# Optimization experiments

Hardware: AMD Instinct MI355X
Metric: run time of the kernel (lower is better)

Reference implementation:

```python
import jax, jax.numpy as jnp
import numpy as np

SC = np.float32(np.sqrt(0.5))


def _reflect_idx(l, m):
    # symmetric-extension gather indices for a length-l axis padded by m each side
    x = np.arange(-m, l + m, dtype=np.float64)
    minx, maxx = -0.5, l - 0.5
    rng = maxx - minx
    mod = np.fmod(x - minx, 2.0 * rng)
    mod = np.where(mod < 0, mod + 2.0 * rng, mod)
    out = np.where(mod >= rng, 2.0 * rng - mod, mod) + minx
    return out.astype(np.int32)


def _conv_h(X, h):
    # true 'valid' convolution (filter flipped, as np.convolve) along H of (N,C,H,W)
    k = h.shape[0]
    w = jnp.flip(h).reshape(1, 1, k, 1).astype(X.dtype)
    N, C, H, W = X.shape
    y = jax.lax.conv_general_dilated(X.reshape(N * C, 1, H, W), w, (1, 1), 'VALID',
                                     dimension_numbers=('NCHW', 'OIHW', 'NCHW'))
    return y.reshape(N, C, -1, W)


def colfilter(X, h):
    # odd-tap filter along rows (H) with symmetric padding, output same H
    m = h.shape[0] // 2
    xe = _reflect_idx(X.shape[2], m)
    return _conv_h(X[:, :, xe], h)


def rowfilter(X, h):
    return colfilter(X.transpose(0, 1, 3, 2), h).transpose(0, 1, 3, 2)


def colifilt(X, ha, hb, highpass):
    # Polyphase form of dtcwt's colifilt: four phase outputs interleaved into 2*H rows.
    N, C, r, W = X.shape
    m = ha.shape[0]
    m2 = m // 2
    xe = _reflect_idx(r, m2)  # len r + m
    hao, hae = ha[0::2], ha[1::2]
    hbo, hbe = hb[0::2], hb[1::2]
    if m2 % 2 == 0:
        t = np.arange(3, r + m, 2)
        off = 2
    else:
        t = np.arange(2, r + m - 1, 2)
        off = 0
    # highpass pairs have sum(ha*hb) < 0 -> swapped quarter-sample phases
    ta, tb = (t - 1, t) if highpass else (t, t - 1)
    Xb = X[:, :, xe[tb - off]]
    Xa = X[:, :, xe[ta - off]]
    Xb2 = X[:, :, xe[tb]] if off else Xb
    Xa2 = X[:, :, xe[ta]] if off else Xa
    y0 = _conv_h(Xb, hao)
    y1 = _conv_h(Xa, hbo)
    y2 = _conv_h(Xb2, hae)
    y3 = _conv_h(Xa2, hbe)
    Y = jnp.stack([y0, y1, y2, y3], axis=3)  # (N,C,r/2,4,W)
    return Y.reshape(N, C, 2 * r, W)


def rowifilt(X, ha, hb, highpass):
    return colifilt(X.transpose(0, 1, 3, 2), ha, hb, highpass).transpose(0, 1, 3, 2)


def c2q(w1, w2):
    # complex orientation pair (N,C,h,w,2) -> real quad image (N,C,2h,2w)
    w1r, w1i = w1[..., 0], w1[..., 1]
    w2r, w2i = w2[..., 0], w2[..., 1]
    x1 = (w1r + w2r) * SC  # top-left
    x2 = (w1i + w2i) * SC  # top-right
    x3 = (w1i - w2i) * SC  # bottom-left
    x4 = (w2r - w1r) * SC  # bottom-right
    N, C, H, W = x1.shape
    top = jnp.stack([x1, x2], axis=-1).reshape(N, C, H, 2 * W)
    bot = jnp.stack([x3, x4], axis=-1).reshape(N, C, H, 2 * W)
    return jnp.stack([top, bot], axis=3).reshape(N, C, 2 * H, 2 * W)


def _bands(yh):
    lh = c2q(yh[:, :, 0], yh[:, :, 5])
    hl = c2q(yh[:, :, 2], yh[:, :, 3])
    hh = c2q(yh[:, :, 1], yh[:, :, 4])
    return lh, hl, hh


def _crop(ll, ref):
    if ll.shape[2] != ref.shape[2]:
        ll = ll[:, :, 1:-1]
    if ll.shape[3] != ref.shape[3]:
        ll = ll[:, :, :, 1:-1]
    return ll


def _inv_j2plus(ll, yh, g0a, g0b, g1a, g1b):
    lh, hl, hh = _bands(yh)
    ll = _crop(ll, lh)
    y1 = colifilt(ll, g0b, g0a, False) + colifilt(lh, g1b, g1a, True)
    y2 = colifilt(hl, g0b, g0a, False) + colifilt(hh, g1b, g1a, True)
    return rowifilt(y1, g0b, g0a, False) + rowifilt(y2, g1b, g1a, True)


def _inv_j1(ll, yh, g0o, g1o):
    lh, hl, hh = _bands(yh)
    ll = _crop(ll, lh)
    y1 = colfilter(ll, g0o) + colfilter(lh, g1o)
    y2 = colfilter(hl, g0o) + colfilter(hh, g1o)
    return rowfilter(y1, g0o) + rowfilter(y2, g1o)


def _filters():
    # near_sym_a (5,7)-tap biorthogonal synthesis filters
    g0o = np.array([-3.0, -15.0, 73.0, 170.0, 73.0, -15.0, -3.0]) / 280.0
    g1o = np.array([-1.0, -5.0, 12.0, -5.0, -1.0]) / 20.0
    # qshift_06 10-tap quarter-shift filters
    h0a = np.array([0.03516384, 0.0, -0.08832942, 0.23389032, 0.76027237,
                    0.58751830, 0.0, -0.11430184, 0.0, 0.0])
    g0b = h0a
    g0a = h0a[::-1]
    g1a = h0a * np.array([1.0, -1.0] * 5)
    g1b = g1a[::-1]
    f32 = lambda a: jnp.asarray(np.ascontiguousarray(a), dtype=jnp.float32)
    return f32(g0o), f32(g1o), f32(g0a), f32(g0b), f32(g1a), f32(g1b)


def setup_inputs():
    key = jax.random.key(0)
    k1, k2, k3, k4 = jax.random.split(key, 4)
    N, C = 4, 64
    yl = jax.random.normal(k1, (N, C, 64, 64), dtype=jnp.float32)
    yh1 = jax.random.normal(k2, (N, C, 6, 128, 128, 2), dtype=jnp.float32)
    yh2 = jax.random.normal(k3, (N, C, 6, 64, 64, 2), dtype=jnp.float32)
    yh3 = jax.random.normal(k4, (N, C, 6, 32, 32, 2), dtype=jnp.float32)
    g0o, g1o, g0a, g0b, g1a, g1b = _filters()
    return {"yl": yl, "yh1": yh1, "yh2": yh2, "yh3": yh3,
            "g0o": g0o, "g1o": g1o, "g0a": g0a, "g0b": g0b, "g1a": g1a, "g1b": g1b}


def reference(yl, yh1, yh2, yh3, g0o, g1o, g0a, g0b, g1a, g1b):
    ll = _inv_j2plus(yl, yh3, g0a, g0b, g1a, g1b)   # 64 -> 128
    ll = _inv_j2plus(ll, yh2, g0a, g0b, g1a, g1b)   # 128 -> 256
    return _inv_j1(ll, yh1, g0o, g1o)               # 256 -> 256
```

## Files before the change

### kernel.cpp

```cpp
#include <hip/hip_runtime.h>

#define SC 0.70710678118654752440f

typedef _Float16 h4v __attribute__((ext_vector_type(4)));
typedef _Float16 h8v __attribute__((ext_vector_type(8)));

__device__ __forceinline__ float rfl(float x) {
    return __int_as_float(__builtin_amdgcn_readfirstlane(__float_as_int(x)));
}

__device__ __forceinline__ float4 ld4(const float* __restrict__ p) {
    return *(const float4*)p;
}
__device__ __forceinline__ float4 ld4(const _Float16* __restrict__ p) {
    h4v h = *(const h4v*)p;
    return make_float4((float)h[0], (float)h[1], (float)h[2], (float)h[3]);
}
__device__ __forceinline__ void st4(float* __restrict__ p, float4 v) {
    *(float4*)p = v;
}
__device__ __forceinline__ void st4(_Float16* __restrict__ p, float4 v) {
    h4v h;
    h[0] = (_Float16)v.x; h[1] = (_Float16)v.y;
    h[2] = (_Float16)v.z; h[3] = (_Float16)v.w;
    *(h4v*)p = h;
}

__device__ __forceinline__ h8v pack8(float4 a, float4 b) {
    h8v h;
    h[0] = (_Float16)a.x; h[1] = (_Float16)a.y;
    h[2] = (_Float16)a.z; h[3] = (_Float16)a.w;
    h[4] = (_Float16)b.x; h[5] = (_Float16)b.y;
    h[6] = (_Float16)b.z; h[7] = (_Float16)b.w;
    return h;
}
__device__ __forceinline__ void unpack8(h8v h, bool rv, float4& y1, float4& y2) {
    float4 p = make_float4((float)h[0], (float)h[1], (float)h[2], (float)h[3]);
    float4 q = make_float4((float)h[4], (float)h[5], (float)h[6], (float)h[7]);
    float4 pr = make_float4(p.w, p.z, p.y, p.x);
    float4 qr = make_float4(q.w, q.z, q.y, q.x);
    y1 = rv ? pr : p;
    y2 = rv ? qr : q;
}

__device__ __forceinline__ int reflFull(int p, int n) {
    int x = max(p, ~p);
    return min(x, 2 * n - 1 - x);
}
__device__ __forceinline__ int pairRefl(int t, int NP, bool& sw) {
    int x = max(t, ~t);
    int tp = min(x, 2 * NP - 1 - x);
    sw = (tp != t);
    return tp;
}

__device__ __forceinline__ constexpr int cflIdx(int s, int k) {
    return (s == 0) ? 8 - 2 * k : (s == 1) ? 1 + 2 * k : (s == 2) ? 9 - 2 * k : 2 * k;
}
__device__ __forceinline__ constexpr int cfhIdx(int s, int k) {
    return (s == 0) ? 1 + 2 * k : (s == 1) ? 8 - 2 * k : (s == 2) ? 2 * k : 9 - 2 * k;
}

__device__ __forceinline__ float4 f4fma(float c, float4 a, float4 acc) {
    return make_float4(fmaf(c, a.x, acc.x), fmaf(c, a.y, acc.y),
                       fmaf(c, a.z, acc.z), fmaf(c, a.w, acc.w));
}
__device__ __forceinline__ float4 f4sel(bool sw, float4 a, float4 b) {
    return sw ? a : b;
}

struct Band4 { float4 e05, o05, e23, o23, e14, o14; };

__device__ __forceinline__ Band4 loadBands4(const float* __restrict__ bp, int HW2,
                                            int boff, bool sw) {
    float4 B0 = *(const float4*)(bp + 0 * HW2 + boff);
    float4 B1 = *(const float4*)(bp + 1 * HW2 + boff);
    float4 B2 = *(const float4*)(bp + 2 * HW2 + boff);
    float4 B3 = *(const float4*)(bp + 3 * HW2 + boff);
    float4 B4 = *(const float4*)(bp + 4 * HW2 + boff);
    float4 B5 = *(const float4*)(bp + 5 * HW2 + boff);
    float4 ve05 = {B0.x + B5.x, B0.y + B5.y, B0.z + B5.z, B0.w + B5.w};
    float4 vo05 = {B0.y - B5.y, B5.x - B0.x, B0.w - B5.w, B5.z - B0.z};
    float4 ve23 = {B2.x + B3.x, B2.y + B3.y, B2.z + B3.z, B2.w + B3.w};
    float4 vo23 = {B2.y - B3.y, B3.x - B2.x, B2.w - B3.w, B3.z - B2.z};
    float4 ve14 = {B1.x + B4.x, B1.y + B4.y, B1.z + B4.z, B1.w + B4.w};
    float4 vo14 = {B1.y - B4.y, B4.x - B1.x, B1.w - B4.w, B4.z - B1.z};
    Band4 r;
    r.e05 = f4sel(sw, vo05, ve05);  r.o05 = f4sel(sw, ve05, vo05);
    r.e23 = f4sel(sw, vo23, ve23);  r.o23 = f4sel(sw, ve23, vo23);
    r.e14 = f4sel(sw, vo14, ve14);  r.o14 = f4sel(sw, ve14, vo14);
    return r;
}

template <int N> struct Log2 { static constexpr int v = 1 + Log2<N / 2>::v; };
template <> struct Log2<1> { static constexpr int v = 0; };

template <int H, int W, bool BND, typename TIn, typename SY>
__device__ __forceinline__ void j2_colstage(
        const TIn* __restrict__ llp, const float* __restrict__ bp,
        const float* G0, const float* G1, SY& sY, int tid, int q0) {
    constexpr int LOGW = Log2<W>::v;
    constexpr int U4 = W / 2, LOGU4 = LOGW - 1;
    constexpr int r = 2 * H, LOGC2 = LOGW + 1;
    constexpr int HW2 = H * W * 2;
    int u4 = tid & (U4 - 1);
    int qq = tid >> LOGU4;
    int q = q0 + qq;
    float4 A1[4], A1b[4], A2[4];
#pragma unroll
    for (int s = 0; s < 4; ++s) {
        A1[s] = {0, 0, 0, 0}; A1b[s] = {0, 0, 0, 0}; A2[s] = {0, 0, 0, 0};
    }
#pragma unroll
    for (int k = 0; k < 5; ++k) {
        int t = q + k - 2;
        int pe, po, tp; bool sw;
        if constexpr (BND) {
            pe = reflFull(2 * t, r);
            po = reflFull(2 * t + 1, r);
            tp = pairRefl(t, H, sw);
        } else {
            pe = 2 * t; po = 2 * t + 1; tp = t; sw = false;
        }
        float4 lle = ld4(llp + ((pe << LOGC2) + 4 * u4));
        float4 llo = ld4(llp + ((po << LOGC2) + 4 * u4));
        Band4 B = loadBands4(bp, HW2, (tp << (LOGW + 1)) + 4 * u4, sw);
#pragma unroll
        for (int s = 0; s < 4; ++s) {
            float4 lv  = (s & 1) ? llo   : lle;
            float4 v05 = (s & 1) ? B.e05 : B.o05;
            float4 v23 = (s & 1) ? B.o23 : B.e23;
            float4 v14 = (s & 1) ? B.e14 : B.o14;
            float c0 = G0[cflIdx(s, k)];
            float c1 = G1[cfhIdx(s, k)];
            A1[s]  = f4fma(c0, lv,  A1[s]);
            A1b[s] = f4fma(c1, v05, A1b[s]);
            A2[s]  = f4fma(c0, v23, f4fma(c1, v14, A2[s]));
        }
    }
#pragma unroll
    for (int s = 0; s < 4; ++s) {
        float4 w1 = f4fma(SC, A1b[s], A1[s]);
        float4 w2 = {SC * A2[s].x, SC * A2[s].y, SC * A2[s].z, SC * A2[s].w};
        sY[4 * qq + s][u4] = pack8(w1, w2);
    }
}

template <int H, int W, typename TIn, typename TOut>
__global__ __launch_bounds__(256) void j2_fused(
        const TIn* __restrict__ ll, const float* __restrict__ yh,
        const float* __restrict__ g0b, const float* __restrict__ g1a,
        TOut* __restrict__ out) {
    constexpr int LOGW = Log2<W>::v;
    constexpr int U4 = W / 2, LOGU4 = LOGW - 1;
    constexpr int QI = 256 / U4;
    constexpr int TI = 4 * QI;
    constexpr int r = 2 * H, COUT = 4 * W;
    constexpr int HW2 = H * W * 2;
    constexpr int NCH = W / 2;
    __shared__ h8v sY[TI][NCH + 1];

    const int tid = threadIdx.x;
    const int nc = blockIdx.y;
    const int q0 = blockIdx.x * QI;
    const TIn* llp = ll + (size_t)nc * r * (2 * W);
    const float* bp  = yh + (size_t)nc * 6 * HW2;

    float G0[10], G1[10];
#pragma unroll
    for (int i = 0; i < 10; ++i) { G0[i] = rfl(g0b[i]); G1[i] = rfl(g1a[i]); }

    if (q0 >= 2 && q0 + QI + 2 <= H)
        j2_colstage<H, W, false>(llp, bp, G0, G1, sY, tid, q0);
    else
        j2_colstage<H, W, true>(llp, bp, G0, G1, sY, tid, q0);
    __syncthreads();

    TOut* op = out + (size_t)nc * (4 * H) * COUT;
#pragma unroll
    for (int v = 0; v < (TI * W) / 512; ++v) {
        int lin = v * 256 + tid;
        int uc = lin & (U4 - 1);
        int il = lin >> LOGU4;
        float e1[6], o1[6], e2[6], o2[6];
#pragma unroll
        for (int d = 0; d < 3; ++d) {
            int a = uc - 1 + d;
            int ac = reflFull(a, NCH);
            bool rv = (ac != a);
            float4 y1, y2;
            unpack8(sY[il][ac], rv, y1, y2);
            e1[2 * d] = y1.x;  o1[2 * d] = y1.y;
            e1[2 * d + 1] = y1.z;  o1[2 * d + 1] = y1.w;
            e2[2 * d] = y2.x;  o2[2 * d] = y2.y;
            e2[2 * d + 1] = y2.z;  o2[2 * d + 1] = y2.w;
        }
        float acc[8];
#pragma unroll
        for (int b = 0; b < 2; ++b)
#pragma unroll
            for (int s = 0; s < 4; ++s) {
                float a = 0.f;
#pragma unroll
                for (int k = 0; k < 5; ++k) {
                    int m = b + k;
                    float v1 = (s & 1) ? o1[m] : e1[m];
                    float v2 = (s & 1) ? e2[m] : o2[m];
                    a = fmaf(G0[cflIdx(s, k)], v1, a);
                    a = fmaf(G1[cfhIdx(s, k)], v2, a);
                }
                acc[4 * b + s] = a;
            }
        int grow = 4 * q0 + il;
        st4(op + (size_t)grow * COUT + 8 * uc,
            make_float4(acc[0], acc[1], acc[2], acc[3]));
        st4(op + (size_t)grow * COUT + 8 * uc + 4,
            make_float4(acc[4], acc[5], acc[6], acc[7]));
    }
}

template <int H, int W, bool BND, typename TIn, typename SY>
__device__ __forceinline__ void j1_colstage(
        const TIn* __restrict__ llp, const float* __restrict__ bp,
        const float* g0f, const float* g1f, SY& sY, int tid, int qi0) {
    constexpr int LOGW = Log2<W>::v;
    constexpr int U4 = W / 2, LOGU4 = LOGW - 1;
    constexpr int r = 2 * H, LOGC2 = LOGW + 1;
    constexpr int HW2 = H * W * 2;
    int u4 = tid & (U4 - 1);
    int qq = tid >> LOGU4;
    int qi = qi0 + qq;
    float4 A1[4], A1b[4], A2[4];
#pragma unroll
    for (int s = 0; s < 4; ++s) {
        A1[s] = {0, 0, 0, 0}; A1b[s] = {0, 0, 0, 0}; A2[s] = {0, 0, 0, 0};
    }
#pragma unroll
    for (int rr = 0; rr < 10; ++rr) {
        int praw = 4 * qi - 3 + rr;
        int p = BND ? reflFull(praw, r) : praw;
        float4 v = ld4(llp + ((p << LOGC2) + 4 * u4));
#pragma unroll
        for (int di = 0; di < 4; ++di) {
            int k = rr - di;
            if (k >= 0 && k <= 6) A1[di] = f4fma(g0f[k], v, A1[di]);
        }
    }
#pragma unroll
    for (int tr = 0; tr < 6; ++tr) {
        int t = 2 * qi - 2 + tr;
        int tp; bool sw;
        if constexpr (BND) tp = pairRefl(t, H, sw);
        else { tp = t; sw = false; }
        Band4 B = loadBands4(bp, HW2, (tp << (LOGW + 1)) + 4 * u4, sw);
#pragma unroll
        for (int di = 0; di < 4; ++di) {
            int k1e = 2 * tr - di - 2;
            int k1o = k1e + 1;
            int k0e = 2 * tr - di - 1;
            int k0o = k0e + 1;
            if (k1e >= 0 && k1e <= 4) {
                A1b[di] = f4fma(g1f[k1e], B.e05, A1b[di]);
                A2[di]  = f4fma(g1f[k1e], B.e14, A2[di]);
            }
            if (k1o >= 0 && k1o <= 4) {
                A1b[di] = f4fma(g1f[k1o], B.o05, A1b[di]);
                A2[di]  = f4fma(g1f[k1o], B.o14, A2[di]);
            }
            if (k0e >= 0 && k0e <= 6) A2[di] = f4fma(g0f[k0e], B.e23, A2[di]);
            if (k0o >= 0 && k0o <= 6) A2[di] = f4fma(g0f[k0o], B.o23, A2[di]);
        }
    }
#pragma unroll
    for (int di = 0; di < 4; ++di) {
        float4 w1 = f4fma(SC, A1b[di], A1[di]);
        float4 w2 = {SC * A2[di].x, SC * A2[di].y, SC * A2[di].z, SC * A2[di].w};
        sY[4 * qq + di][u4] = pack8(w1, w2);
    }
}

template <int H, int W, typename TIn>
__global__ __launch_bounds__(256) void j1_fused(
        const TIn* __restrict__ ll, const float* __restrict__ yh,
        const float* __restrict__ g0o, const float* __restrict__ g1o,
        float* __restrict__ out) {
    constexpr int LOGW = Log2<W>::v;
    constexpr int U4 = W / 2, LOGU4 = LOGW - 1;
    constexpr int QI = 256 / U4;
    constexpr int TI = 4 * QI;
    constexpr int r = 2 * H, c = 2 * W;
    constexpr int HW2 = H * W * 2;
    constexpr int NCH = W / 2;
    __shared__ h8v sY[TI][NCH + 1];

    const int tid = threadIdx.x;
    const int nc = blockIdx.y;
    const int qi0 = blockIdx.x * QI;
    const TIn* llp = ll + (size_t)nc * r * c;
    const float* bp  = yh + (size_t)nc * 6 * HW2;

    float g0f[7], g1f[5];
#pragma unroll
    for (int k = 0; k < 7; ++k) g0f[k] = rfl(g0o[6 - k]);
#pragma unroll
    for (int k = 0; k < 5; ++k) g1f[k] = rfl(g1o[4 - k]);

    if (qi0 >= 1 && 2 * (qi0 + QI) + 4 <= H && 4 * (qi0 + QI) + 7 <= r)
        j1_colstage<H, W, false>(llp, bp, g0f, g1f, sY, tid, qi0);
    else
        j1_colstage<H, W, true>(llp, bp, g0f, g1f, sY, tid, qi0);
    __syncthreads();

    float* op = out + (size_t)nc * r * c;
#pragma unroll
    for (int v = 0; v < (TI * W) / 1024; ++v) {
        int lin = v * 256 + tid;
        int g8 = lin & (W / 4 - 1);
        int il = lin >> (LOGW - 2);
        float e1[8], o1[8], e2[8], o2[8];
#pragma unroll
        for (int d = 0; d < 4; ++d) {
            int a = 2 * g8 - 1 + d;
            int ac = reflFull(a, NCH);
            bool rv = (ac != a);
            float4 y1, y2;
            unpack8(sY[il][ac], rv, y1, y2);
            e1[2 * d] = y1.x;  o1[2 * d] = y1.y;
            e1[2 * d + 1] = y1.z;  o1[2 * d + 1] = y1.w;
            e2[2 * d] = y2.x;  o2[2 * d] = y2.y;
            e2[2 * d + 1] = y2.z;  o2[2 * d + 1] = y2.w;
        }
        float acc[8];
#pragma unroll
        for (int b = 0; b < 2; ++b)
#pragma unroll
            for (int s = 0; s < 4; ++s) {
                float a = 0.f;
#pragma unroll
                for (int k = 0; k < 7; ++k) {
                    int rel = s + k + 1;
                    int mm = (rel >> 1) + 2 * b;
                    a = fmaf(g0f[k], (rel & 1) ? o1[mm] : e1[mm], a);
                }
#pragma unroll
                for (int k = 0; k < 5; ++k) {
                    int rel = s + k + 2;
                    int mm = (rel >> 1) + 2 * b;
                    a = fmaf(g1f[k], (rel & 1) ? o2[mm] : e2[mm], a);
                }
                acc[4 * b + s] = a;
            }
        int grow = 4 * qi0 + il;
        *(float4*)(op + (size_t)grow * c + 8 * g8) =
            make_float4(acc[0], acc[1], acc[2], acc[3]);
        *(float4*)(op + (size_t)grow * c + 8 * g8 + 4) =
            make_float4(acc[4], acc[5], acc[6], acc[7]);
    }
}

extern "C" void kernel_launch(void* const* d_in, const int* in_sizes, int n_in,
                              void* d_out, int out_size, void* d_ws, size_t ws_size,
                              hipStream_t stream) {
    const float* yl  = (const float*)d_in[0];
    const float* yh1 = (const float*)d_in[1];
    const float* yh2 = (const float*)d_in[2];
    const float* yh3 = (const float*)d_in[3];
    const float* g0o = (const float*)d_in[4];
    const float* g1o = (const float*)d_in[5];
    const float* g0b = (const float*)d_in[7];
    const float* g1a = (const float*)d_in[8];
    float* out = (float*)d_out;

    const int NC = 256;
    char* ws = (char*)d_ws;
    _Float16* llA = (_Float16*)ws;
    _Float16* llB = (_Float16*)(ws + ((size_t)16 << 20));

    j2_fused<32, 32, float, _Float16><<<dim3(2, NC), 256, 0, stream>>>(
        yl, yh3, g0b, g1a, llA);
    j2_fused<64, 64, _Float16, _Float16><<<dim3(8, NC), 256, 0, stream>>>(
        llA, yh2, g0b, g1a, llB);
    j1_fused<128, 128, _Float16><<<dim3(16, NC), 256, 0, stream>>>(
        llB, yh1, g0o, g1o, out);
}
```

Before: 100.4 us.

## Split column stage into two accumulator passes and fold sqrt(0.5) into filters

The column stage now runs in two sequential passes: one accumulating the A2 band combination (bands 1-4) and writing the upper half of each shared slot, then one accumulating A1 (lowpass plus bands 0/5) into the lower half. Only four float4 accumulators are live at a time instead of twelve, and the sqrt(0.5) scale is folded into precomputed scaled filter taps, which removes the final scaling multiplies. Launch bounds now request 5 waves per SIMD to take advantage of the lower register pressure. The cost is that the band-index and reflection arithmetic for the shared rows is recomputed in each pass, and the stores become two half-width writes.

```diff
diff --git a/kernel.cpp b/kernel.cpp
--- a/kernel.cpp
+++ b/kernel.cpp
@@ -25,13 +25,10 @@
     h[2] = (_Float16)v.z; h[3] = (_Float16)v.w;
     *(h4v*)p = h;
 }
-
-__device__ __forceinline__ h8v pack8(float4 a, float4 b) {
-    h8v h;
-    h[0] = (_Float16)a.x; h[1] = (_Float16)a.y;
-    h[2] = (_Float16)a.z; h[3] = (_Float16)a.w;
-    h[4] = (_Float16)b.x; h[5] = (_Float16)b.y;
-    h[6] = (_Float16)b.z; h[7] = (_Float16)b.w;
+__device__ __forceinline__ h4v toh4(float4 v) {
+    h4v h;
+    h[0] = (_Float16)v.x; h[1] = (_Float16)v.y;
+    h[2] = (_Float16)v.z; h[3] = (_Float16)v.w;
     return h;
 }
 __device__ __forceinline__ void unpack8(h8v h, bool rv, float4& y1, float4& y2) {
@@ -68,28 +65,11 @@
 __device__ __forceinline__ float4 f4sel(bool sw, float4 a, float4 b) {
     return sw ? a : b;
 }
-
-struct Band4 { float4 e05, o05, e23, o23, e14, o14; };
-
-__device__ __forceinline__ Band4 loadBands4(const float* __restrict__ bp, int HW2,
-                                            int boff, bool sw) {
-    float4 B0 = *(const float4*)(bp + 0 * HW2 + boff);
-    float4 B1 = *(const float4*)(bp + 1 * HW2 + boff);
-    float4 B2 = *(const float4*)(bp + 2 * HW2 + boff);
-    float4 B3 = *(const float4*)(bp + 3 * HW2 + boff);
-    float4 B4 = *(const float4*)(bp + 4 * HW2 + boff);
-    float4 B5 = *(const float4*)(bp + 5 * HW2 + boff);
-    float4 ve05 = {B0.x + B5.x, B0.y + B5.y, B0.z + B5.z, B0.w + B5.w};
-    float4 vo05 = {B0.y - B5.y, B5.x - B0.x, B0.w - B5.w, B5.z - B0.z};
-    float4 ve23 = {B2.x + B3.x, B2.y + B3.y, B2.z + B3.z, B2.w + B3.w};
-    float4 vo23 = {B2.y - B3.y, B3.x - B2.x, B2.w - B3.w, B3.z - B2.z};
-    float4 ve14 = {B1.x + B4.x, B1.y + B4.y, B1.z + B4.z, B1.w + B4.w};
-    float4 vo14 = {B1.y - B4.y, B4.x - B1.x, B1.w - B4.w, B4.z - B1.z};
-    Band4 r;
-    r.e05 = f4sel(sw, vo05, ve05);  r.o05 = f4sel(sw, ve05, vo05);
-    r.e23 = f4sel(sw, vo23, ve23);  r.o23 = f4sel(sw, ve23, vo23);
-    r.e14 = f4sel(sw, vo14, ve14);  r.o14 = f4sel(sw, ve14, vo14);
-    return r;
+__device__ __forceinline__ float4 f4add(float4 a, float4 b) {
+    return make_float4(a.x + b.x, a.y + b.y, a.z + b.z, a.w + b.w);
+}
+__device__ __forceinline__ float4 oSub(float4 A, float4 B) {
+    return make_float4(A.y - B.y, B.x - A.x, A.w - B.w, B.z - A.z);
 }
 
 template <int N> struct Log2 { static constexpr int v = 1 + Log2<N / 2>::v; };
@@ -98,56 +78,83 @@
 template <int H, int W, bool BND, typename TIn, typename SY>
 __device__ __forceinline__ void j2_colstage(
         const TIn* __restrict__ llp, const float* __restrict__ bp,
-        const float* G0, const float* G1, SY& sY, int tid, int q0) {
+        const float* G0, const float* SG0, const float* SG1,
+        SY& sY, int tid, int q0) {
     constexpr int LOGW = Log2<W>::v;
     constexpr int U4 = W / 2, LOGU4 = LOGW - 1;
     constexpr int r = 2 * H, LOGC2 = LOGW + 1;
     constexpr int HW2 = H * W * 2;
-    int u4 = tid & (U4 - 1);
-    int qq = tid >> LOGU4;
-    int q = q0 + qq;
-    float4 A1[4], A1b[4], A2[4];
-#pragma unroll
-    for (int s = 0; s < 4; ++s) {
-        A1[s] = {0, 0, 0, 0}; A1b[s] = {0, 0, 0, 0}; A2[s] = {0, 0, 0, 0};
-    }
-#pragma unroll
-    for (int k = 0; k < 5; ++k) {
-        int t = q + k - 2;
-        int pe, po, tp; bool sw;
-        if constexpr (BND) {
-            pe = reflFull(2 * t, r);
-            po = reflFull(2 * t + 1, r);
-            tp = pairRefl(t, H, sw);
-        } else {
-            pe = 2 * t; po = 2 * t + 1; tp = t; sw = false;
-        }
-        float4 lle = ld4(llp + ((pe << LOGC2) + 4 * u4));
-        float4 llo = ld4(llp + ((po << LOGC2) + 4 * u4));
-        Band4 B = loadBands4(bp, HW2, (tp << (LOGW + 1)) + 4 * u4, sw);
-#pragma unroll
-        for (int s = 0; s < 4; ++s) {
-            float4 lv  = (s & 1) ? llo   : lle;
-            float4 v05 = (s & 1) ? B.e05 : B.o05;
-            float4 v23 = (s & 1) ? B.o23 : B.e23;
-            float4 v14 = (s & 1) ? B.e14 : B.o14;
-            float c0 = G0[cflIdx(s, k)];
-            float c1 = G1[cfhIdx(s, k)];
-            A1[s]  = f4fma(c0, lv,  A1[s]);
-            A1b[s] = f4fma(c1, v05, A1b[s]);
-            A2[s]  = f4fma(c0, v23, f4fma(c1, v14, A2[s]));
-        }
-    }
-#pragma unroll
-    for (int s = 0; s < 4; ++s) {
-        float4 w1 = f4fma(SC, A1b[s], A1[s]);
-        float4 w2 = {SC * A2[s].x, SC * A2[s].y, SC * A2[s].z, SC * A2[s].w};
-        sY[4 * qq + s][u4] = pack8(w1, w2);
+    const int u4 = tid & (U4 - 1);
+    const int qq = tid >> LOGU4;
+    const int q = q0 + qq;
+
+    {
+        float4 A2[4];
+#pragma unroll
+        for (int s = 0; s < 4; ++s) A2[s] = {0, 0, 0, 0};
+#pragma unroll
+        for (int k = 0; k < 5; ++k) {
+            int t = q + k - 2;
+            int tp; bool sw;
+            if constexpr (BND) tp = pairRefl(t, H, sw);
+            else { tp = t; sw = false; }
+            int boff = (tp << (LOGW + 1)) + 4 * u4;
+            float4 B1 = *(const float4*)(bp + 1 * HW2 + boff);
+            float4 B2 = *(const float4*)(bp + 2 * HW2 + boff);
+            float4 B3 = *(const float4*)(bp + 3 * HW2 + boff);
+            float4 B4 = *(const float4*)(bp + 4 * HW2 + boff);
+            float4 ve23 = f4add(B2, B3), vo23 = oSub(B2, B3);
+            float4 ve14 = f4add(B1, B4), vo14 = oSub(B1, B4);
+            float4 e23 = f4sel(sw, vo23, ve23), o23 = f4sel(sw, ve23, vo23);
+            float4 e14 = f4sel(sw, vo14, ve14), o14 = f4sel(sw, ve14, vo14);
+#pragma unroll
+            for (int s = 0; s < 4; ++s) {
+                float4 v23 = (s & 1) ? o23 : e23;
+                float4 v14 = (s & 1) ? e14 : o14;
+                A2[s] = f4fma(SG0[cflIdx(s, k)], v23,
+                        f4fma(SG1[cfhIdx(s, k)], v14, A2[s]));
+            }
+        }
+#pragma unroll
+        for (int s = 0; s < 4; ++s)
+            ((h4v*)&sY[4 * qq + s][u4])[1] = toh4(A2[s]);
+    }
+    {
+        float4 A1[4];
+#pragma unroll
+        for (int s = 0; s < 4; ++s) A1[s] = {0, 0, 0, 0};
+#pragma unroll
+        for (int k = 0; k < 5; ++k) {
+            int t = q + k - 2;
+            int pe, po, tp; bool sw;
+            if constexpr (BND) {
+                pe = reflFull(2 * t, r);
+                po = reflFull(2 * t + 1, r);
+                tp = pairRefl(t, H, sw);
+            } else { pe = 2 * t; po = 2 * t + 1; tp = t; sw = false; }
+            float4 lle = ld4(llp + ((pe << LOGC2) + 4 * u4));
+            float4 llo = ld4(llp + ((po << LOGC2) + 4 * u4));
+            int boff = (tp << (LOGW + 1)) + 4 * u4;
+            float4 B0 = *(const float4*)(bp + 0 * HW2 + boff);
+            float4 B5 = *(const float4*)(bp + 5 * HW2 + boff);
+            float4 ve05 = f4add(B0, B5), vo05 = oSub(B0, B5);
+            float4 e05 = f4sel(sw, vo05, ve05), o05 = f4sel(sw, ve05, vo05);
+#pragma unroll
+            for (int s = 0; s < 4; ++s) {
+                float4 lv  = (s & 1) ? llo : lle;
+                float4 v05 = (s & 1) ? e05 : o05;
+                A1[s] = f4fma(G0[cflIdx(s, k)], lv,
+                        f4fma(SG1[cfhIdx(s, k)], v05, A1[s]));
+            }
+        }
+#pragma unroll
+        for (int s = 0; s < 4; ++s)
+            ((h4v*)&sY[4 * qq + s][u4])[0] = toh4(A1[s]);
     }
 }
 
 template <int H, int W, typename TIn, typename TOut>
-__global__ __launch_bounds__(256) void j2_fused(
+__global__ __launch_bounds__(256, 5) void j2_fused(
         const TIn* __restrict__ ll, const float* __restrict__ yh,
         const float* __restrict__ g0b, const float* __restrict__ g1a,
         TOut* __restrict__ out) {
@@ -166,14 +173,17 @@
     const TIn* llp = ll + (size_t)nc * r * (2 * W);
     const float* bp  = yh + (size_t)nc * 6 * HW2;
 
-    float G0[10], G1[10];
-#pragma unroll
-    for (int i = 0; i < 10; ++i) { G0[i] = rfl(g0b[i]); G1[i] = rfl(g1a[i]); }
+    float G0[10], G1[10], SG0[10], SG1[10];
+#pragma unroll
+    for (int i = 0; i < 10; ++i) {
+        G0[i] = rfl(g0b[i]); G1[i] = rfl(g1a[i]);
+        SG0[i] = rfl(SC * G0[i]); SG1[i] = rfl(SC * G1[i]);
+    }
 
     if (q0 >= 2 && q0 + QI + 2 <= H)
-        j2_colstage<H, W, false>(llp, bp, G0, G1, sY, tid, q0);
+        j2_colstage<H, W, false>(llp, bp, G0, SG0, SG1, sY, tid, q0);
     else
-        j2_colstage<H, W, true>(llp, bp, G0, G1, sY, tid, q0);
+        j2_colstage<H, W, true>(llp, bp, G0, SG0, SG1, sY, tid, q0);
     __syncthreads();
 
     TOut* op = out + (size_t)nc * (4 * H) * COUT;
@@ -222,65 +232,93 @@
 template <int H, int W, bool BND, typename TIn, typename SY>
 __device__ __forceinline__ void j1_colstage(
         const TIn* __restrict__ llp, const float* __restrict__ bp,
-        const float* g0f, const float* g1f, SY& sY, int tid, int qi0) {
+        const float* g0f, const float* Sg0f, const float* Sg1f,
+        SY& sY, int tid, int qi0) {
     constexpr int LOGW = Log2<W>::v;
     constexpr int U4 = W / 2, LOGU4 = LOGW - 1;
     constexpr int r = 2 * H, LOGC2 = LOGW + 1;
     constexpr int HW2 = H * W * 2;
-    int u4 = tid & (U4 - 1);
-    int qq = tid >> LOGU4;
-    int qi = qi0 + qq;
-    float4 A1[4], A1b[4], A2[4];
-#pragma unroll
-    for (int s = 0; s < 4; ++s) {
-        A1[s] = {0, 0, 0, 0}; A1b[s] = {0, 0, 0, 0}; A2[s] = {0, 0, 0, 0};
-    }
-#pragma unroll
-    for (int rr = 0; rr < 10; ++rr) {
-        int praw = 4 * qi - 3 + rr;
-        int p = BND ? reflFull(praw, r) : praw;
-        float4 v = ld4(llp + ((p << LOGC2) + 4 * u4));
-#pragma unroll
-        for (int di = 0; di < 4; ++di) {
-            int k = rr - di;
-            if (k >= 0 && k <= 6) A1[di] = f4fma(g0f[k], v, A1[di]);
-        }
-    }
-#pragma unroll
-    for (int tr = 0; tr < 6; ++tr) {
-        int t = 2 * qi - 2 + tr;
-        int tp; bool sw;
-        if constexpr (BND) tp = pairRefl(t, H, sw);
-        else { tp = t; sw = false; }
-        Band4 B = loadBands4(bp, HW2, (tp << (LOGW + 1)) + 4 * u4, sw);
-#pragma unroll
-        for (int di = 0; di < 4; ++di) {
-            int k1e = 2 * tr - di - 2;
-            int k1o = k1e + 1;
-            int k0e = 2 * tr - di - 1;
-            int k0o = k0e + 1;
-            if (k1e >= 0 && k1e <= 4) {
-                A1b[di] = f4fma(g1f[k1e], B.e05, A1b[di]);
-                A2[di]  = f4fma(g1f[k1e], B.e14, A2[di]);
-            }
-            if (k1o >= 0 && k1o <= 4) {
-                A1b[di] = f4fma(g1f[k1o], B.o05, A1b[di]);
-                A2[di]  = f4fma(g1f[k1o], B.o14, A2[di]);
-            }
-            if (k0e >= 0 && k0e <= 6) A2[di] = f4fma(g0f[k0e], B.e23, A2[di]);
-            if (k0o >= 0 && k0o <= 6) A2[di] = f4fma(g0f[k0o], B.o23, A2[di]);
-        }
-    }
-#pragma unroll
-    for (int di = 0; di < 4; ++di) {
-        float4 w1 = f4fma(SC, A1b[di], A1[di]);
-        float4 w2 = {SC * A2[di].x, SC * A2[di].y, SC * A2[di].z, SC * A2[di].w};
-        sY[4 * qq + di][u4] = pack8(w1, w2);
+    const int u4 = tid & (U4 - 1);
+    const int qq = tid >> LOGU4;
+    const int qi = qi0 + qq;
+
+    {
+        float4 A2[4];
+#pragma unroll
+        for (int s = 0; s < 4; ++s) A2[s] = {0, 0, 0, 0};
+#pragma unroll
+        for (int tr = 0; tr < 6; ++tr) {
+            int t = 2 * qi - 2 + tr;
+            int tp; bool sw;
+            if constexpr (BND) tp = pairRefl(t, H, sw);
+            else { tp = t; sw = false; }
+            int boff = (tp << (LOGW + 1)) + 4 * u4;
+            float4 B1 = *(const float4*)(bp + 1 * HW2 + boff);
+            float4 B2 = *(const float4*)(bp + 2 * HW2 + boff);
+            float4 B3 = *(const float4*)(bp + 3 * HW2 + boff);
+            float4 B4 = *(const float4*)(bp + 4 * HW2 + boff);
+            float4 ve23 = f4add(B2, B3), vo23 = oSub(B2, B3);
+            float4 ve14 = f4add(B1, B4), vo14 = oSub(B1, B4);
+            float4 e23 = f4sel(sw, vo23, ve23), o23 = f4sel(sw, ve23, vo23);
+            float4 e14 = f4sel(sw, vo14, ve14), o14 = f4sel(sw, ve14, vo14);
+#pragma unroll
+            for (int di = 0; di < 4; ++di) {
+                int k1e = 2 * tr - di - 2;
+                int k1o = k1e + 1;
+                int k0e = 2 * tr - di - 1;
+                int k0o = k0e + 1;
+                if (k1e >= 0 && k1e <= 4) A2[di] = f4fma(Sg1f[k1e], e14, A2[di]);
+                if (k1o >= 0 && k1o <= 4) A2[di] = f4fma(Sg1f[k1o], o14, A2[di]);
+                if (k0e >= 0 && k0e <= 6) A2[di] = f4fma(Sg0f[k0e], e23, A2[di]);
+                if (k0o >= 0 && k0o <= 6) A2[di] = f4fma(Sg0f[k0o], o23, A2[di]);
+            }
+        }
+#pragma unroll
+        for (int di = 0; di < 4; ++di)
+            ((h4v*)&sY[4 * qq + di][u4])[1] = toh4(A2[di]);
+    }
+    {
+        float4 A1[4];
+#pragma unroll
+        for (int s = 0; s < 4; ++s) A1[s] = {0, 0, 0, 0};
+#pragma unroll
+        for (int rr = 0; rr < 10; ++rr) {
+            int praw = 4 * qi - 3 + rr;
+            int p = BND ? reflFull(praw, r) : praw;
+            float4 v = ld4(llp + ((p << LOGC2) + 4 * u4));
+#pragma unroll
+            for (int di = 0; di < 4; ++di) {
+                int k = rr - di;
+                if (k >= 0 && k <= 6) A1[di] = f4fma(g0f[k], v, A1[di]);
+            }
+        }
+#pragma unroll
+        for (int tr = 0; tr < 6; ++tr) {
+            int t = 2 * qi - 2 + tr;
+            int tp; bool sw;
+            if constexpr (BND) tp = pairRefl(t, H, sw);
+            else { tp = t; sw = false; }
+            int boff = (tp << (LOGW + 1)) + 4 * u4;
+            float4 B0 = *(const float4*)(bp + 0 * HW2 + boff);
+            float4 B5 = *(const float4*)(bp + 5 * HW2 + boff);
+            float4 ve05 = f4add(B0, B5), vo05 = oSub(B0, B5);
+            float4 e05 = f4sel(sw, vo05, ve05), o05 = f4sel(sw, ve05, vo05);
+#pragma unroll
+            for (int di = 0; di < 4; ++di) {
+                int k1e = 2 * tr - di - 2;
+                int k1o = k1e + 1;
+                if (k1e >= 0 && k1e <= 4) A1[di] = f4fma(Sg1f[k1e], e05, A1[di]);
+                if (k1o >= 0 && k1o <= 4) A1[di] = f4fma(Sg1f[k1o], o05, A1[di]);
+            }
+        }
+#pragma unroll
+        for (int di = 0; di < 4; ++di)
+            ((h4v*)&sY[4 * qq + di][u4])[0] = toh4(A1[di]);
     }
 }
 
 template <int H, int W, typename TIn>
-__global__ __launch_bounds__(256) void j1_fused(
+__global__ __launch_bounds__(256, 5) void j1_fused(
         const TIn* __restrict__ ll, const float* __restrict__ yh,
         const float* __restrict__ g0o, const float* __restrict__ g1o,
         float* __restrict__ out) {
@@ -299,16 +337,20 @@
     const TIn* llp = ll + (size_t)nc * r * c;
     const float* bp  = yh + (size_t)nc * 6 * HW2;
 
-    float g0f[7], g1f[5];
-#pragma unroll
-    for (int k = 0; k < 7; ++k) g0f[k] = rfl(g0o[6 - k]);
-#pragma unroll
-    for (int k = 0; k < 5; ++k) g1f[k] = rfl(g1o[4 - k]);
+    float g0f[7], g1f[5], Sg0f[7], Sg1f[5];
+#pragma unroll
+    for (int k = 0; k < 7; ++k) {
+        g0f[k] = rfl(g0o[6 - k]); Sg0f[k] = rfl(SC * g0f[k]);
+    }
+#pragma unroll
+    for (int k = 0; k < 5; ++k) {
+        g1f[k] = rfl(g1o[4 - k]); Sg1f[k] = rfl(SC * g1f[k]);
+    }
 
     if (qi0 >= 1 && 2 * (qi0 + QI) + 4 <= H && 4 * (qi0 + QI) + 7 <= r)
-        j1_colstage<H, W, false>(llp, bp, g0f, g1f, sY, tid, qi0);
+        j1_colstage<H, W, false>(llp, bp, g0f, Sg0f, Sg1f, sY, tid, qi0);
     else
-        j1_colstage<H, W, true>(llp, bp, g0f, g1f, sY, tid, qi0);
+        j1_colstage<H, W, true>(llp, bp, g0f, Sg0f, Sg1f, sY, tid, qi0);
     __syncthreads();
 
     float* op = out + (size_t)nc * r * c;
```

After: 325.2 us. 224% more time.

## Halve per-thread column width in column stages and double block count

Applied to the files above, without the earlier changes.

Each thread in the column stage now handles two complex columns (float2) instead of four, so a block covers half as many row quads and twice as many blocks are launched. This is meant to raise occupancy and latency hiding across the GPU, at the cost of narrower 8-byte loads and more redundant filter-tap setup per block. Shared memory writes become two half2 stores per cell instead of one h8 store. The j1 stage also folds the SC scale into the highpass coefficients, removing the separate A1b accumulator and the final scale multiplies.

```diff
diff --git a/kernel.cpp b/kernel.cpp
--- a/kernel.cpp
+++ b/kernel.cpp
@@ -2,6 +2,7 @@
 
 #define SC 0.70710678118654752440f
 
+typedef _Float16 h2v __attribute__((ext_vector_type(2)));
 typedef _Float16 h4v __attribute__((ext_vector_type(4)));
 typedef _Float16 h8v __attribute__((ext_vector_type(8)));
 
@@ -9,12 +10,12 @@
     return __int_as_float(__builtin_amdgcn_readfirstlane(__float_as_int(x)));
 }
 
-__device__ __forceinline__ float4 ld4(const float* __restrict__ p) {
-    return *(const float4*)p;
-}
-__device__ __forceinline__ float4 ld4(const _Float16* __restrict__ p) {
-    h4v h = *(const h4v*)p;
-    return make_float4((float)h[0], (float)h[1], (float)h[2], (float)h[3]);
+__device__ __forceinline__ float2 ld2(const float* __restrict__ p) {
+    return *(const float2*)p;
+}
+__device__ __forceinline__ float2 ld2(const _Float16* __restrict__ p) {
+    h2v h = *(const h2v*)p;
+    return make_float2((float)h[0], (float)h[1]);
 }
 __device__ __forceinline__ void st4(float* __restrict__ p, float4 v) {
     *(float4*)p = v;
@@ -25,13 +26,9 @@
     h[2] = (_Float16)v.z; h[3] = (_Float16)v.w;
     *(h4v*)p = h;
 }
-
-__device__ __forceinline__ h8v pack8(float4 a, float4 b) {
-    h8v h;
-    h[0] = (_Float16)a.x; h[1] = (_Float16)a.y;
-    h[2] = (_Float16)a.z; h[3] = (_Float16)a.w;
-    h[4] = (_Float16)b.x; h[5] = (_Float16)b.y;
-    h[6] = (_Float16)b.z; h[7] = (_Float16)b.w;
+__device__ __forceinline__ h2v toh2(float2 v) {
+    h2v h;
+    h[0] = (_Float16)v.x; h[1] = (_Float16)v.y;
     return h;
 }
 __device__ __forceinline__ void unpack8(h8v h, bool rv, float4& y1, float4& y2) {
@@ -61,34 +58,30 @@
     return (s == 0) ? 1 + 2 * k : (s == 1) ? 8 - 2 * k : (s == 2) ? 2 * k : 9 - 2 * k;
 }
 
-__device__ __forceinline__ float4 f4fma(float c, float4 a, float4 acc) {
-    return make_float4(fmaf(c, a.x, acc.x), fmaf(c, a.y, acc.y),
-                       fmaf(c, a.z, acc.z), fmaf(c, a.w, acc.w));
-}
-__device__ __forceinline__ float4 f4sel(bool sw, float4 a, float4 b) {
+__device__ __forceinline__ float2 f2fma(float c, float2 a, float2 acc) {
+    return make_float2(fmaf(c, a.x, acc.x), fmaf(c, a.y, acc.y));
+}
+__device__ __forceinline__ float2 f2sel(bool sw, float2 a, float2 b) {
     return sw ? a : b;
 }
 
-struct Band4 { float4 e05, o05, e23, o23, e14, o14; };
-
-__device__ __forceinline__ Band4 loadBands4(const float* __restrict__ bp, int HW2,
+struct Band2 { float2 e05, o05, e23, o23, e14, o14; };
+
+__device__ __forceinline__ Band2 loadBands2(const float* __restrict__ bp, int HW2,
                                             int boff, bool sw) {
-    float4 B0 = *(const float4*)(bp + 0 * HW2 + boff);
-    float4 B1 = *(const float4*)(bp + 1 * HW2 + boff);
-    float4 B2 = *(const float4*)(bp + 2 * HW2 + boff);
-    float4 B3 = *(const float4*)(bp + 3 * HW2 + boff);
-    float4 B4 = *(const float4*)(bp + 4 * HW2 + boff);
-    float4 B5 = *(const float4*)(bp + 5 * HW2 + boff);
-    float4 ve05 = {B0.x + B5.x, B0.y + B5.y, B0.z + B5.z, B0.w + B5.w};
-    float4 vo05 = {B0.y - B5.y, B5.x - B0.x, B0.w - B5.w, B5.z - B0.z};
-    float4 ve23 = {B2.x + B3.x, B2.y + B3.y, B2.z + B3.z, B2.w + B3.w};
-    float4 vo23 = {B2.y - B3.y, B3.x - B2.x, B2.w - B3.w, B3.z - B2.z};
-    float4 ve14 = {B1.x + B4.x, B1.y + B4.y, B1.z + B4.z, B1.w + B4.w};
-    float4 vo14 = {B1.y - B4.y, B4.x - B1.x, B1.w - B4.w, B4.z - B1.z};
-    Band4 r;
-    r.e05 = f4sel(sw, vo05, ve05);  r.o05 = f4sel(sw, ve05, vo05);
-    r.e23 = f4sel(sw, vo23, ve23);  r.o23 = f4sel(sw, ve23, vo23);
-    r.e14 = f4sel(sw, vo14, ve14);  r.o14 = f4sel(sw, ve14, vo14);
+    float2 B0 = *(const float2*)(bp + 0 * HW2 + boff);
+    float2 B1 = *(const float2*)(bp + 1 * HW2 + boff);
+    float2 B2 = *(const float2*)(bp + 2 * HW2 + boff);
+    float2 B3 = *(const float2*)(bp + 3 * HW2 + boff);
+    float2 B4 = *(const float2*)(bp + 4 * HW2 + boff);
+    float2 B5 = *(const float2*)(bp + 5 * HW2 + boff);
+    float2 ve05 = {B0.x + B5.x, B0.y + B5.y}, vo05 = {B0.y - B5.y, B5.x - B0.x};
+    float2 ve23 = {B2.x + B3.x, B2.y + B3.y}, vo23 = {B2.y - B3.y, B3.x - B2.x};
+    float2 ve14 = {B1.x + B4.x, B1.y + B4.y}, vo14 = {B1.y - B4.y, B4.x - B1.x};
+    Band2 r;
+    r.e05 = f2sel(sw, vo05, ve05);  r.o05 = f2sel(sw, ve05, vo05);
+    r.e23 = f2sel(sw, vo23, ve23);  r.o23 = f2sel(sw, ve23, vo23);
+    r.e14 = f2sel(sw, vo14, ve14);  r.o14 = f2sel(sw, ve14, vo14);
     return r;
 }
 
@@ -100,16 +93,15 @@
         const TIn* __restrict__ llp, const float* __restrict__ bp,
         const float* G0, const float* G1, SY& sY, int tid, int q0) {
     constexpr int LOGW = Log2<W>::v;
-    constexpr int U4 = W / 2, LOGU4 = LOGW - 1;
     constexpr int r = 2 * H, LOGC2 = LOGW + 1;
     constexpr int HW2 = H * W * 2;
-    int u4 = tid & (U4 - 1);
-    int qq = tid >> LOGU4;
-    int q = q0 + qq;
-    float4 A1[4], A1b[4], A2[4];
+    const int u2 = tid & (W - 1);
+    const int qq = tid >> LOGW;
+    const int q = q0 + qq;
+    float2 A1[4], A1b[4], A2[4];
 #pragma unroll
     for (int s = 0; s < 4; ++s) {
-        A1[s] = {0, 0, 0, 0}; A1b[s] = {0, 0, 0, 0}; A2[s] = {0, 0, 0, 0};
+        A1[s] = {0, 0}; A1b[s] = {0, 0}; A2[s] = {0, 0};
     }
 #pragma unroll
     for (int k = 0; k < 5; ++k) {
@@ -119,30 +111,30 @@
             pe = reflFull(2 * t, r);
             po = reflFull(2 * t + 1, r);
             tp = pairRefl(t, H, sw);
-        } else {
-            pe = 2 * t; po = 2 * t + 1; tp = t; sw = false;
-        }
-        float4 lle = ld4(llp + ((pe << LOGC2) + 4 * u4));
-        float4 llo = ld4(llp + ((po << LOGC2) + 4 * u4));
-        Band4 B = loadBands4(bp, HW2, (tp << (LOGW + 1)) + 4 * u4, sw);
+        } else { pe = 2 * t; po = 2 * t + 1; tp = t; sw = false; }
+        float2 lle = ld2(llp + ((pe << LOGC2) + 2 * u2));
+        float2 llo = ld2(llp + ((po << LOGC2) + 2 * u2));
+        Band2 B = loadBands2(bp, HW2, (tp << (LOGW + 1)) + 2 * u2, sw);
 #pragma unroll
         for (int s = 0; s < 4; ++s) {
-            float4 lv  = (s & 1) ? llo   : lle;
-            float4 v05 = (s & 1) ? B.e05 : B.o05;
-            float4 v23 = (s & 1) ? B.o23 : B.e23;
-            float4 v14 = (s & 1) ? B.e14 : B.o14;
+            float2 lv  = (s & 1) ? llo   : lle;
+            float2 v05 = (s & 1) ? B.e05 : B.o05;
+            float2 v23 = (s & 1) ? B.o23 : B.e23;
+            float2 v14 = (s & 1) ? B.e14 : B.o14;
             float c0 = G0[cflIdx(s, k)];
             float c1 = G1[cfhIdx(s, k)];
-            A1[s]  = f4fma(c0, lv,  A1[s]);
-            A1b[s] = f4fma(c1, v05, A1b[s]);
-            A2[s]  = f4fma(c0, v23, f4fma(c1, v14, A2[s]));
+            A1[s]  = f2fma(c0, lv,  A1[s]);
+            A1b[s] = f2fma(c1, v05, A1b[s]);
+            A2[s]  = f2fma(c0, v23, f2fma(c1, v14, A2[s]));
         }
     }
 #pragma unroll
     for (int s = 0; s < 4; ++s) {
-        float4 w1 = f4fma(SC, A1b[s], A1[s]);
-        float4 w2 = {SC * A2[s].x, SC * A2[s].y, SC * A2[s].z, SC * A2[s].w};
-        sY[4 * qq + s][u4] = pack8(w1, w2);
+        float2 w1 = f2fma(SC, A1b[s], A1[s]);
+        float2 w2 = {SC * A2[s].x, SC * A2[s].y};
+        _Float16* cell = (_Float16*)&sY[4 * qq + s][u2 >> 1];
+        ((h2v*)cell)[u2 & 1]       = toh2(w1);
+        ((h2v*)cell)[2 + (u2 & 1)] = toh2(w2);
     }
 }
 
@@ -153,7 +145,7 @@
         TOut* __restrict__ out) {
     constexpr int LOGW = Log2<W>::v;
     constexpr int U4 = W / 2, LOGU4 = LOGW - 1;
-    constexpr int QI = 256 / U4;
+    constexpr int QI = 256 / W;
     constexpr int TI = 4 * QI;
     constexpr int r = 2 * H, COUT = 4 * W;
     constexpr int HW2 = H * W * 2;
@@ -222,28 +214,26 @@
 template <int H, int W, bool BND, typename TIn, typename SY>
 __device__ __forceinline__ void j1_colstage(
         const TIn* __restrict__ llp, const float* __restrict__ bp,
-        const float* g0f, const float* g1f, SY& sY, int tid, int qi0) {
+        const float* g0f, const float* Sg0f, const float* Sg1f,
+        SY& sY, int tid, int qi0) {
     constexpr int LOGW = Log2<W>::v;
-    constexpr int U4 = W / 2, LOGU4 = LOGW - 1;
     constexpr int r = 2 * H, LOGC2 = LOGW + 1;
     constexpr int HW2 = H * W * 2;
-    int u4 = tid & (U4 - 1);
-    int qq = tid >> LOGU4;
-    int qi = qi0 + qq;
-    float4 A1[4], A1b[4], A2[4];
-#pragma unroll
-    for (int s = 0; s < 4; ++s) {
-        A1[s] = {0, 0, 0, 0}; A1b[s] = {0, 0, 0, 0}; A2[s] = {0, 0, 0, 0};
-    }
+    const int u2 = tid & (W - 1);
+    const int qq = tid >> LOGW;
+    const int qi = qi0 + qq;
+    float2 A1[4], A2[4];
+#pragma unroll
+    for (int s = 0; s < 4; ++s) { A1[s] = {0, 0}; A2[s] = {0, 0}; }
 #pragma unroll
     for (int rr = 0; rr < 10; ++rr) {
         int praw = 4 * qi - 3 + rr;
         int p = BND ? reflFull(praw, r) : praw;
-        float4 v = ld4(llp + ((p << LOGC2) + 4 * u4));
+        float2 v = ld2(llp + ((p << LOGC2) + 2 * u2));
 #pragma unroll
         for (int di = 0; di < 4; ++di) {
             int k = rr - di;
-            if (k >= 0 && k <= 6) A1[di] = f4fma(g0f[k], v, A1[di]);
+            if (k >= 0 && k <= 6) A1[di] = f2fma(g0f[k], v, A1[di]);
         }
     }
 #pragma unroll
@@ -252,7 +242,7 @@
         int tp; bool sw;
         if constexpr (BND) tp = pairRefl(t, H, sw);
         else { tp = t; sw = false; }
-        Band4 B = loadBands4(bp, HW2, (tp << (LOGW + 1)) + 4 * u4, sw);
+        Band2 B = loadBands2(bp, HW2, (tp << (LOGW + 1)) + 2 * u2, sw);
 #pragma unroll
         for (int di = 0; di < 4; ++di) {
             int k1e = 2 * tr - di - 2;
@@ -260,22 +250,22 @@
             int k0e = 2 * tr - di - 1;
             int k0o = k0e + 1;
             if (k1e >= 0 && k1e <= 4) {
-                A1b[di] = f4fma(g1f[k1e], B.e05, A1b[di]);
-                A2[di]  = f4fma(g1f[k1e], B.e14, A2[di]);
+                A1[di] = f2fma(Sg1f[k1e], B.e05, A1[di]);
+                A2[di] = f2fma(Sg1f[k1e], B.e14, A2[di]);
             }
             if (k1o >= 0 && k1o <= 4) {
-                A1b[di] = f4fma(g1f[k1o], B.o05, A1b[di]);
-                A2[di]  = f4fma(g1f[k1o], B.o14, A2[di]);
+                A1[di] = f2fma(Sg1f[k1o], B.o05, A1[di]);
+                A2[di] = f2fma(Sg1f[k1o], B.o14, A2[di]);
             }
-            if (k0e >= 0 && k0e <= 6) A2[di] = f4fma(g0f[k0e], B.e23, A2[di]);
-            if (k0o >= 0 && k0o <= 6) A2[di] = f4fma(g0f[k0o], B.o23, A2[di]);
+            if (k0e >= 0 && k0e <= 6) A2[di] = f2fma(Sg0f[k0e], B.e23, A2[di]);
+            if (k0o >= 0 && k0o <= 6) A2[di] = f2fma(Sg0f[k0o], B.o23, A2[di]);
         }
     }
 #pragma unroll
     for (int di = 0; di < 4; ++di) {
-        float4 w1 = f4fma(SC, A1b[di], A1[di]);
-        float4 w2 = {SC * A2[di].x, SC * A2[di].y, SC * A2[di].z, SC * A2[di].w};
-        sY[4 * qq + di][u4] = pack8(w1, w2);
+        _Float16* cell = (_Float16*)&sY[4 * qq + di][u2 >> 1];
+        ((h2v*)cell)[u2 & 1]       = toh2(A1[di]);
+        ((h2v*)cell)[2 + (u2 & 1)] = toh2(A2[di]);
     }
 }
 
@@ -285,8 +275,7 @@
         const float* __restrict__ g0o, const float* __restrict__ g1o,
         float* __restrict__ out) {
     constexpr int LOGW = Log2<W>::v;
-    constexpr int U4 = W / 2, LOGU4 = LOGW - 1;
-    constexpr int QI = 256 / U4;
+    constexpr int QI = 256 / W;
     constexpr int TI = 4 * QI;
     constexpr int r = 2 * H, c = 2 * W;
     constexpr int HW2 = H * W * 2;
@@ -299,16 +288,20 @@
     const TIn* llp = ll + (size_t)nc * r * c;
     const float* bp  = yh + (size_t)nc * 6 * HW2;
 
-    float g0f[7], g1f[5];
-#pragma unroll
-    for (int k = 0; k < 7; ++k) g0f[k] = rfl(g0o[6 - k]);
-#pragma unroll
-    for (int k = 0; k < 5; ++k) g1f[k] = rfl(g1o[4 - k]);
+    float g0f[7], g1f[5], Sg0f[7], Sg1f[5];
+#pragma unroll
+    for (int k = 0; k < 7; ++k) {
+        g0f[k] = rfl(g0o[6 - k]); Sg0f[k] = rfl(SC * g0f[k]);
+    }
+#pragma unroll
+    for (int k = 0; k < 5; ++k) {
+        g1f[k] = rfl(g1o[4 - k]); Sg1f[k] = rfl(SC * g1f[k]);
+    }
 
     if (qi0 >= 1 && 2 * (qi0 + QI) + 4 <= H && 4 * (qi0 + QI) + 7 <= r)
-        j1_colstage<H, W, false>(llp, bp, g0f, g1f, sY, tid, qi0);
+        j1_colstage<H, W, false>(llp, bp, g0f, Sg0f, Sg1f, sY, tid, qi0);
     else
-        j1_colstage<H, W, true>(llp, bp, g0f, g1f, sY, tid, qi0);
+        j1_colstage<H, W, true>(llp, bp, g0f, Sg0f, Sg1f, sY, tid, qi0);
     __syncthreads();
 
     float* op = out + (size_t)nc * r * c;
@@ -376,10 +369,10 @@
     _Float16* llA = (_Float16*)ws;
     _Float16* llB = (_Float16*)(ws + ((size_t)16 << 20));
 
-    j2_fused<32, 32, float, _Float16><<<dim3(2, NC), 256, 0, stream>>>(
+    j2_fused<32, 32, float, _Float16><<<dim3(4, NC), 256, 0, stream>>>(
         yl, yh3, g0b, g1a, llA);
-    j2_fused<64, 64, _Float16, _Float16><<<dim3(8, NC), 256, 0, stream>>>(
+    j2_fused<64, 64, _Float16, _Float16><<<dim3(16, NC), 256, 0, stream>>>(
         llA, yh2, g0b, g1a, llB);
-    j1_fused<128, 128, _Float16><<<dim3(16, NC), 256, 0, stream>>>(
+    j1_fused<128, 128, _Float16><<<dim3(32, NC), 256, 0, stream>>>(
         llB, yh1, g0o, g1o, out);
 }
```

Result: slower. 112.6 us (+12.2%).
